# Performance work log

Hardware: AMD Instinct MI355X
Metric: run time of the kernel (lower is better)

## Reference

```python
import jax, jax.numpy as jnp
import numpy as np

MUL = 32          # multiplicity of 0e and 1o in edge_messages_irreps
E = 40000         # number of edges
NODE_DIM = 128    # 128x0e node feats
EDGE_DIM = 32     # 32x0e edge feats
WEIGHT_NUMEL = 5 * MUL * MUL  # 5 uvu instructions, (u,v)=(32,32) weights each

# Levi-Civita tensor = sqrt(6) * wigner_3j(1,1,1) in the e3nn real basis
_eps = np.zeros((3, 3, 3), np.float32)
for a, b, c in [(0, 1, 2), (1, 2, 0), (2, 0, 1)]:
    _eps[a, b, c] = 1.0
    _eps[a, c, b] = -1.0
EPS = jnp.asarray(_eps)


def setup_inputs() -> dict:
    key = jax.random.key(0)
    ks = jax.random.split(key, 13)
    return {
        "edge_feats": jax.random.normal(ks[0], (E, EDGE_DIM), jnp.float32),
        "edge_messages1": jax.random.normal(ks[1], (E, 4 * MUL), jnp.float32),
        "edge_messages2": jax.random.normal(ks[2], (E, 4 * MUL), jnp.float32),
        "node_feats_sender": jax.random.normal(ks[3], (E, NODE_DIM), jnp.float32),
        "node_feats_receiver": jax.random.normal(ks[4], (E, NODE_DIM), jnp.float32),
        "W_nodes": jax.random.normal(ks[5], (NODE_DIM, EDGE_DIM), jnp.float32),
        "W_mlp1": jax.random.normal(ks[6], (3 * EDGE_DIM, 128), jnp.float32),
        "W_mlp2": jax.random.normal(ks[7], (128, 128), jnp.float32),
        "W_mlp3": jax.random.normal(ks[8], (128, WEIGHT_NUMEL), jnp.float32),
        "W_out_0e": jax.random.normal(ks[9], (2 * MUL, MUL), jnp.float32),
        "W_out_1o": jax.random.normal(ks[10], (2 * MUL, MUL), jnp.float32),
        "W_out_1e": jax.random.normal(ks[11], (MUL, MUL), jnp.float32),
        "edge_index": jax.random.randint(ks[12], (2, E), 0, 10000, jnp.int64 if jax.config.jax_enable_x64 else jnp.int32),
    }


def reference(edge_feats, edge_messages1, edge_messages2, node_feats_sender,
              node_feats_receiver, W_nodes, W_mlp1, W_mlp2, W_mlp3,
              W_out_0e, W_out_1o, W_out_1e, edge_index):
    # nodes_linear: o3.Linear on pure scalars == dense matmul with 1/sqrt(fan_in)
    s_send = (node_feats_sender @ W_nodes) * (1.0 / np.sqrt(NODE_DIM))
    s_recv = (node_feats_receiver @ W_nodes) * (1.0 / np.sqrt(NODE_DIM))
    scal = jnp.concatenate([s_send, s_recv, edge_feats], axis=1)  # [E, 96]

    # FullyConnectedNet [96,128,128,weight_numel] with SiLU, e3nn fan-in scaling
    h = jax.nn.silu((scal @ W_mlp1) * (1.0 / np.sqrt(3 * EDGE_DIM)))
    h = jax.nn.silu((h @ W_mlp2) * (1.0 / np.sqrt(128)))
    w = (h @ W_mlp3) * (1.0 / np.sqrt(128))          # [E, 5120] per-edge TP weights
    w = w.reshape(-1, 5, MUL, MUL)                    # 5 uvu instructions

    # split messages into 32x0e scalars and 32x1o vectors
    x1_0 = edge_messages1[:, :MUL]
    x1_1 = edge_messages1[:, MUL:].reshape(-1, MUL, 3)
    x2_0 = edge_messages2[:, :MUL]
    x2_1 = edge_messages2[:, MUL:].reshape(-1, MUL, 3)

    # per-edge-weighted uvu tensor product; alpha = sqrt(ir_out.dim / fan) with
    # CG constants (1, d/sqrt(3), eps/sqrt(6)) folded in
    c1 = jnp.einsum('euv,eu,ev->eu', w[:, 0], x1_0, x2_0) * (1.0 / np.sqrt(MUL))          # 0e
    c2 = jnp.einsum('euv,eu,evj->euj', w[:, 1], x1_0, x2_1) * (1.0 / np.sqrt(MUL))        # 1o
    c3 = jnp.einsum('euv,eui,ev->eui', w[:, 2], x1_1, x2_0) * (1.0 / np.sqrt(MUL))        # 1o
    c4 = jnp.einsum('euv,eui,evi->eu', w[:, 3], x1_1, x2_1) * (1.0 / np.sqrt(3 * MUL))    # 0e
    c5 = jnp.einsum('euv,eui,evj,ijk->euk', w[:, 4], x1_1, x2_1, EPS) * (1.0 / np.sqrt(2 * MUL))  # 1e

    # output_linear: o3.Linear over irreps_mid -> 32x0e + 32x1o + 32x1e
    mid_0e = jnp.concatenate([c1, c4], axis=1)        # [E, 64]
    mid_1o = jnp.concatenate([c2, c3], axis=1)        # [E, 64, 3]
    out_0e = (mid_0e @ W_out_0e) * (1.0 / np.sqrt(2 * MUL))                      # [E, 32]
    out_1o = jnp.einsum('euj,uw->ewj', mid_1o, W_out_1o) * (1.0 / np.sqrt(2 * MUL))
    out_1e = jnp.einsum('euk,uw->ewk', c5, W_out_1e) * (1.0 / np.sqrt(MUL))

    n = out_0e.shape[0]
    return jnp.concatenate(
        [out_0e, out_1o.reshape(n, 3 * MUL), out_1e.reshape(n, 3 * MUL)], axis=1)  # [E, 224]
```

## Files before the change

kernel.cpp:

```cpp
#include <hip/hip_runtime.h>
#include <hip/hip_bf16.h>
#include <math.h>

typedef __attribute__((ext_vector_type(8)))  short bf16x8;
typedef __attribute__((ext_vector_type(4)))  float f32x4;
typedef __attribute__((ext_vector_type(16))) float f32x16;

#define S128 0.08838834764831845f
#define S96  0.10206207261596575f
#define S32  0.17677669529663687f
#define S64  0.125f
#define NE   40000

__device__ __forceinline__ float silu_f(float x){ return x / (1.0f + expf(-x)); }
__device__ __forceinline__ ushort f2b(float x){
    __hip_bfloat16 b = __float2bfloat16(x); return *(ushort*)&b;
}
__device__ __forceinline__ float b2f(ushort u){
    return __uint_as_float(((uint)u) << 16);
}
__device__ __forceinline__ uint packbf(float a, float b){
    return (uint)f2b(a) | ((uint)f2b(b) << 16);
}

__global__ __launch_bounds__(256)
void prep_weights(const float* __restrict__ Wn, const float* __restrict__ W1,
                  const float* __restrict__ W2, ushort* __restrict__ WnT,
                  ushort* __restrict__ W1T, ushort* __restrict__ W2T) {
    int idx = blockIdx.x * 256 + threadIdx.x;
    if (idx < 4096) {
        int n = idx >> 7, k = idx & 127;
        WnT[n * 128 + k] = f2b(Wn[k * 32 + n]);
    } else if (idx < 16384) {
        int t = idx - 4096; int n = t / 96, k = t - n * 96;
        W1T[n * 96 + k] = f2b(W1[k * 128 + n]);
    } else {
        int t = idx - 16384; int n = t >> 7, k = t & 127;
        W2T[n * 128 + k] = f2b(W2[k * 128 + n]);
    }
}

__global__ __launch_bounds__(256)
void w3_fragpack(const float* __restrict__ W3, ushort* __restrict__ w3A) {
    const int pu = blockIdx.x;
    const int t  = threadIdx.x;
    #pragma unroll
    for (int s = 0; s < 2; ++s) {
        int slot = s * 256 + t;
        int ks = slot >> 6, l = slot & 63;
        int m = pu * 32 + (l & 31);
        int kbase = ks * 16 + (l >> 5) * 8;
        bf16x8 v;
        #pragma unroll
        for (int i = 0; i < 8; ++i)
            v[i] = (short)f2b(W3[(size_t)(kbase + i) * 5120 + m]);
        *(bf16x8*)&w3A[((size_t)(pu * 8 + ks) * 64 + l) * 8] = v;
    }
}

__global__ __launch_bounds__(512, 6)
void mega6(const float* __restrict__ ef,  const float* __restrict__ em2,
           const float* __restrict__ nfs, const float* __restrict__ nfr,
           const ushort* __restrict__ WnT, const ushort* __restrict__ W1T,
           const ushort* __restrict__ W2T, const ushort* __restrict__ w3A,
           ushort* __restrict__ dt)
{
    __shared__ __align__(16) ushort scratch[16640];
    __shared__ __align__(16) ushort hbuf[64 * 128];

    const int tid  = threadIdx.x;
    const int lane = tid & 63, wv = tid >> 6;
    const int l15  = lane & 15, lg = lane >> 4;
    const int e0   = blockIdx.x * 64;

    ushort* scal = scratch;
    ushort* h1b  = scratch + 6656;
    float*  x2f  = (float*)scratch;

    #pragma unroll
    for (int q = 0; q < 4; ++q) {
        int idx = q * 512 + tid;
        int e = idx >> 5, j = idx & 31;
        scal[e * 104 + 64 + j] = f2b(ef[(size_t)(e0 + e) * 32 + j]);
    }

    {
        const int h = wv >> 2, eb = (wv & 3) * 16;
        const float* src = h ? nfr : nfs;
        const size_t erow = (size_t)(e0 + eb + l15) * 128;
        f32x4 acc1[2] = {{0,0,0,0},{0,0,0,0}};
        #pragma unroll
        for (int ks = 0; ks < 4; ++ks) {
            float4 va = *(const float4*)(src + erow + ks * 32 + lg * 8);
            float4 vb = *(const float4*)(src + erow + ks * 32 + lg * 8 + 4);
            bf16x8 a;
            a[0]=(short)f2b(va.x); a[1]=(short)f2b(va.y);
            a[2]=(short)f2b(va.z); a[3]=(short)f2b(va.w);
            a[4]=(short)f2b(vb.x); a[5]=(short)f2b(vb.y);
            a[6]=(short)f2b(vb.z); a[7]=(short)f2b(vb.w);
            #pragma unroll
            for (int nf = 0; nf < 2; ++nf) {
                bf16x8 b = *(const bf16x8*)(WnT + (nf * 16 + l15) * 128 + ks * 32 + lg * 8);
                acc1[nf] = __builtin_amdgcn_mfma_f32_16x16x32_bf16(a, b, acc1[nf], 0, 0, 0);
            }
        }
        #pragma unroll
        for (int nf = 0; nf < 2; ++nf)
            #pragma unroll
            for (int r = 0; r < 4; ++r)
                scal[(eb + lg * 4 + r) * 104 + h * 32 + nf * 16 + l15] =
                    f2b(acc1[nf][r] * S128);
    }
    __syncthreads();

    {
        const int et = wv & 3, nh = wv >> 2;
        f32x4 acc2[4] = {{0,0,0,0},{0,0,0,0},{0,0,0,0},{0,0,0,0}};
        #pragma unroll
        for (int ks = 0; ks < 3; ++ks) {
            bf16x8 a = *(const bf16x8*)&scal[(et * 16 + l15) * 104 + ks * 32 + lg * 8];
            #pragma unroll
            for (int nf = 0; nf < 4; ++nf) {
                int gn = nh * 4 + nf;
                bf16x8 b = *(const bf16x8*)(W1T + (gn * 16 + l15) * 96 + ks * 32 + lg * 8);
                acc2[nf] = __builtin_amdgcn_mfma_f32_16x16x32_bf16(a, b, acc2[nf], 0, 0, 0);
            }
        }
        #pragma unroll
        for (int nf = 0; nf < 4; ++nf)
            #pragma unroll
            for (int r = 0; r < 4; ++r)
                h1b[(et * 16 + lg * 4 + r) * 136 + (nh * 4 + nf) * 16 + l15] =
                    f2b(silu_f(acc2[nf][r] * S96));
    }
    __syncthreads();

    {
        const int et = wv & 3, nh = wv >> 2;
        f32x4 acc3[4] = {{0,0,0,0},{0,0,0,0},{0,0,0,0},{0,0,0,0}};
        #pragma unroll
        for (int ks = 0; ks < 4; ++ks) {
            bf16x8 a = *(const bf16x8*)&h1b[(et * 16 + l15) * 136 + ks * 32 + lg * 8];
            #pragma unroll
            for (int nf = 0; nf < 4; ++nf) {
                int gn = nh * 4 + nf;
                bf16x8 b = *(const bf16x8*)(W2T + (gn * 16 + l15) * 128 + ks * 32 + lg * 8);
                acc3[nf] = __builtin_amdgcn_mfma_f32_16x16x32_bf16(a, b, acc3[nf], 0, 0, 0);
            }
        }
        __syncthreads();
        #pragma unroll
        for (int nf = 0; nf < 4; ++nf)
            #pragma unroll
            for (int r = 0; r < 4; ++r) {
                int e = et * 16 + lg * 4 + r;
                int col = (nh * 4 + nf) * 16 + l15;
                hbuf[e * 128 + (col ^ ((e & 15) << 3))] =
                    f2b(silu_f(acc3[nf][r] * S128));
            }
    }

    {
        int e = tid >> 3, grp = tid & 7;
        const float* xr = em2 + (size_t)(e0 + e) * 128;
        float* dst = &x2f[e * 130];
        #pragma unroll
        for (int r = 0; r < 16; ++r) {
            int idx = grp * 16 + r;
            int reg = idx & 15;
            int vb = (reg & 3) + 8 * (reg >> 2);
            float val;
            if (idx < 32) {
                int hi2 = idx >> 4;
                val = xr[vb + 4 * hi2];
            } else {
                int slot = (idx - 32) >> 4;
                int j = slot >> 1, hi2 = slot & 1;
                val = xr[32 + (vb + 4 * hi2) * 3 + j];
            }
            dst[idx] = val;
        }
    }
    __syncthreads();

    const int el  = lane & 31;
    const int hi  = lane >> 5;
    const int sw0 = (el & 15) << 3;
    const float* x2r0 = &x2f[el * 130];
    const float* x2r1 = &x2f[(32 + el) * 130];

    #pragma unroll 1
    for (int un = 0; un < 20; ++un) {
        const int pu = un * 8 + wv;
        const int p = pu >> 5, u = pu & 31;
        const ushort* Ab = w3A + (size_t)pu * 4096 + lane * 8;

        bf16x8 a[8];
        #pragma unroll
        for (int ks = 0; ks < 8; ++ks)
            a[ks] = *(const bf16x8*)(Ab + ks * 512);

        #pragma unroll 1
        for (int eh = 0; eh < 2; ++eh) {
            const ushort* hrow = &hbuf[(eh * 32 + el) * 128];
            f32x16 acc = {0,0,0,0,0,0,0,0,0,0,0,0,0,0,0,0};
            #pragma unroll
            for (int ks = 0; ks < 8; ++ks) {
                bf16x8 b = *(const bf16x8*)&hrow[(ks * 16 + hi * 8) ^ sw0];
                acc = __builtin_amdgcn_mfma_f32_32x32x16_bf16(a[ks], b, acc, 0, 0, 0);
            }
            const float* xr = eh ? x2r1 : x2r0;
            const int ecol = e0 + eh * 32 + el;
            if (p == 0 || p == 2) {
                float s = 0.f;
                #pragma unroll
                for (int g = 0; g < 8; ++g) {
                    float2 q = *(const float2*)&xr[hi * 16 + g * 2];
                    s += acc[2*g] * q.x + acc[2*g+1] * q.y;
                }
                s += __shfl_xor(s, 32);
                if (hi == 0)
                    dt[(size_t)(((p == 0) ? 0 : 128) + u) * NE + ecol] = f2b(s * S128);
            } else {
                const int row0 = ((p == 1) ? 32 : (p == 3) ? 160 : 256) + u * 3;
                #pragma unroll
                for (int j = 0; j < 3; ++j) {
                    float s = 0.f;
                    #pragma unroll
                    for (int g = 0; g < 8; ++g) {
                        float2 q = *(const float2*)&xr[32 + (j * 2 + hi) * 16 + g * 2];
                        s += acc[2*g] * q.x + acc[2*g+1] * q.y;
                    }
                    s += __shfl_xor(s, 32);
                    if (hi == 0)
                        dt[(size_t)(row0 + j) * NE + ecol] = f2b(s * S128);
                }
            }
        }
    }
}

__global__ __launch_bounds__(256)
void finalize2(const float* __restrict__ em1, const ushort* __restrict__ dt,
               const float* __restrict__ W0e, const float* __restrict__ W1o,
               const float* __restrict__ W1e, float* __restrict__ out)
{
    __shared__ __align__(16) ushort dl[352 * 33];
    __shared__ __align__(16) ushort x1b[32 * 132];
    const int tid  = threadIdx.x;
    const int lane = tid & 63, wv = tid >> 6;
    const int l15  = lane & 15, lg = lane >> 4;
    const int eb   = blockIdx.x * 32;

    for (int idx = tid; idx < 352 * 32; idx += 256) {
        int row = idx >> 5, e = idx & 31;
        dl[row * 33 + e] = dt[(size_t)row * NE + eb + e];
    }
    {
        int e = tid >> 3, seg = tid & 7;
        const float* x1 = em1 + (size_t)(eb + e) * 128 + seg * 16;
        #pragma unroll
        for (int q = 0; q < 4; ++q) {
            float4 v = *(const float4*)(x1 + q * 4);
            *(uint*)&x1b[e * 132 + seg * 16 + q * 4]     = packbf(v.x, v.y);
            *(uint*)&x1b[e * 132 + seg * 16 + q * 4 + 2] = packbf(v.z, v.w);
        }
    }
    __syncthreads();

    #pragma unroll 1
    for (int it = 0; it < 4; ++it) {
        int unit = it * 4 + wv;
        if (unit >= 14) break;
        int mi = unit & 1, task = unit >> 1;
        const int ei = mi * 16 + l15;
        const ushort* xe = &x1b[ei * 132];
        const size_t orow = (size_t)(eb + mi * 16 + lg * 4) * 224;

        if (task == 0) {
            bf16x8 af0, af1;
            #pragma unroll
            for (int t = 0; t < 8; ++t) {
                int u = lg * 8 + t;
                af0[t] = (short)f2b(S32 * b2f(xe[u]) * b2f(dl[u * 33 + ei]));
                float c4 = 0.f;
                #pragma unroll
                for (int i = 0; i < 3; ++i)
                    c4 += b2f(xe[32 + u * 3 + i]) * b2f(dl[(160 + u * 3 + i) * 33 + ei]);
                af1[t] = (short)f2b(c4 * S96);
            }
            #pragma unroll
            for (int nf = 0; nf < 2; ++nf) {
                bf16x8 bf0, bf1;
                #pragma unroll
                for (int t = 0; t < 8; ++t) {
                    bf0[t] = (short)f2b(W0e[(lg * 8 + t) * 32 + nf * 16 + l15]);
                    bf1[t] = (short)f2b(W0e[(32 + lg * 8 + t) * 32 + nf * 16 + l15]);
                }
                f32x4 o = {0.f, 0.f, 0.f, 0.f};
                o = __builtin_amdgcn_mfma_f32_16x16x32_bf16(af0, bf0, o, 0, 0, 0);
                o = __builtin_amdgcn_mfma_f32_16x16x32_bf16(af1, bf1, o, 0, 0, 0);
                #pragma unroll
                for (int rr = 0; rr < 4; ++rr)
                    out[orow + (size_t)rr * 224 + nf * 16 + l15] = o[rr] * S64;
            }
        } else if (task <= 3) {
            int j = task - 1;
            bf16x8 af0, af1;
            #pragma unroll
            for (int t = 0; t < 8; ++t) {
                int u = lg * 8 + t;
                af0[t] = (short)f2b(S32 * b2f(xe[u]) * b2f(dl[(32 + u * 3 + j) * 33 + ei]));
                af1[t] = (short)f2b(S32 * b2f(xe[32 + u * 3 + j]) * b2f(dl[(128 + u) * 33 + ei]));
            }
            #pragma unroll
            for (int nf = 0; nf < 2; ++nf) {
                bf16x8 bf0, bf1;
                #pragma unroll
                for (int t = 0; t < 8; ++t) {
                    bf0[t] = (short)f2b(W1o[(lg * 8 + t) * 32 + nf * 16 + l15]);
                    bf1[t] = (short)f2b(W1o[(32 + lg * 8 + t) * 32 + nf * 16 + l15]);
                }
                f32x4 o = {0.f, 0.f, 0.f, 0.f};
                o = __builtin_amdgcn_mfma_f32_16x16x32_bf16(af0, bf0, o, 0, 0, 0);
                o = __builtin_amdgcn_mfma_f32_16x16x32_bf16(af1, bf1, o, 0, 0, 0);
                #pragma unroll
                for (int rr = 0; rr < 4; ++rr)
                    out[orow + (size_t)rr * 224 + 32 + (nf * 16 + l15) * 3 + j] = o[rr] * S64;
            }
        } else {
            int k = task - 4;
            int k1 = k + 1; if (k1 > 2) k1 -= 3;
            int k2 = k + 2; if (k2 > 2) k2 -= 3;
            bf16x8 af0;
            #pragma unroll
            for (int t = 0; t < 8; ++t) {
                int u = lg * 8 + t;
                float a_ = b2f(xe[32 + u * 3 + k1]) * b2f(dl[(256 + u * 3 + k2) * 33 + ei])
                         - b2f(xe[32 + u * 3 + k2]) * b2f(dl[(256 + u * 3 + k1) * 33 + ei]);
                af0[t] = (short)f2b(a_ * S64);
            }
            #pragma unroll
            for (int nf = 0; nf < 2; ++nf) {
                bf16x8 bf0;
                #pragma unroll
                for (int t = 0; t < 8; ++t)
                    bf0[t] = (short)f2b(W1e[(lg * 8 + t) * 32 + nf * 16 + l15]);
                f32x4 o = {0.f, 0.f, 0.f, 0.f};
                o = __builtin_amdgcn_mfma_f32_16x16x32_bf16(af0, bf0, o, 0, 0, 0);
                #pragma unroll
                for (int rr = 0; rr < 4; ++rr)
                    out[orow + (size_t)rr * 224 + 128 + (nf * 16 + l15) * 3 + k] = o[rr] * S32;
            }
        }
    }
}

extern "C" void kernel_launch(void* const* d_in, const int* in_sizes, int n_in,
                              void* d_out, int out_size, void* d_ws, size_t ws_size,
                              hipStream_t stream) {
    const float* ef  = (const float*)d_in[0];
    const float* em1 = (const float*)d_in[1];
    const float* em2 = (const float*)d_in[2];
    const float* nfs = (const float*)d_in[3];
    const float* nfr = (const float*)d_in[4];
    const float* Wn  = (const float*)d_in[5];
    const float* W1  = (const float*)d_in[6];
    const float* W2  = (const float*)d_in[7];
    const float* W3  = (const float*)d_in[8];
    const float* W0e = (const float*)d_in[9];
    const float* W1o = (const float*)d_in[10];
    const float* W1e = (const float*)d_in[11];
    float* out = (float*)d_out;

    const int E = in_sizes[0] / 32;

    char* ws = (char*)d_ws;
    ushort* w3A = (ushort*)ws;
    size_t off = (size_t)5120 * 128 * 2;
    ushort* WnT = (ushort*)(ws + off);  off += 32 * 128 * 2;
    ushort* W1T = (ushort*)(ws + off);  off += 128 * 96 * 2;
    ushort* W2T = (ushort*)(ws + off);  off += 128 * 128 * 2;
    ushort* dt  = (ushort*)(ws + off);

    prep_weights<<<128, 256, 0, stream>>>(Wn, W1, W2, WnT, W1T, W2T);
    w3_fragpack<<<160, 256, 0, stream>>>(W3, w3A);
    mega6<<<E / 64, 512, 0, stream>>>(ef, em2, nfs, nfr,
                                      WnT, W1T, W2T, w3A, dt);
    finalize2<<<E / 32, 256, 0, stream>>>(em1, dt, W0e, W1o, W1e, out);
}
```

Baseline: 145.0 us.

## Split fused MLP+W3 kernel into two kernels, doubling blocks for the W3 GEMM

The fused kernel is split into an MLP kernel that writes the per-tile h2 activations to a global scratch image, and a GEMM kernel launched with twice as many blocks, each handling half of the 160 (path,u) slices. The S128 scale is folded into the packed W3 weights, and the x2 contraction uses float4 LDS reads with a padded row stride. This aims to raise parallelism and shorten the serial per-block loop, at the cost of an extra global round trip for h2, a recomputed x2 staging per half, and an extra launch.

```diff
diff --git a/kernel.cpp b/kernel.cpp
--- a/kernel.cpp
+++ b/kernel.cpp
@@ -53,29 +53,28 @@
         bf16x8 v;
         #pragma unroll
         for (int i = 0; i < 8; ++i)
-            v[i] = (short)f2b(W3[(size_t)(kbase + i) * 5120 + m]);
+            v[i] = (short)f2b(W3[(size_t)(kbase + i) * 5120 + m] * S128);
         *(bf16x8*)&w3A[((size_t)(pu * 8 + ks) * 64 + l) * 8] = v;
     }
 }
 
 __global__ __launch_bounds__(512, 6)
-void mega6(const float* __restrict__ ef,  const float* __restrict__ em2,
-           const float* __restrict__ nfs, const float* __restrict__ nfr,
-           const ushort* __restrict__ WnT, const ushort* __restrict__ W1T,
-           const ushort* __restrict__ W2T, const ushort* __restrict__ w3A,
-           ushort* __restrict__ dt)
+void mlp_h2(const float* __restrict__ ef,  const float* __restrict__ nfs,
+            const float* __restrict__ nfr, const ushort* __restrict__ WnT,
+            const ushort* __restrict__ W1T, const ushort* __restrict__ W2T,
+            ushort* __restrict__ h2img)
 {
-    __shared__ __align__(16) ushort scratch[16640];
-    __shared__ __align__(16) ushort hbuf[64 * 128];
+    __shared__ __align__(16) ushort scratch[15360];
+    __shared__ __align__(16) ushort h2s[64 * 128];
 
     const int tid  = threadIdx.x;
     const int lane = tid & 63, wv = tid >> 6;
     const int l15  = lane & 15, lg = lane >> 4;
-    const int e0   = blockIdx.x * 64;
+    const int tile = blockIdx.x;
+    const int e0   = tile * 64;
 
     ushort* scal = scratch;
     ushort* h1b  = scratch + 6656;
-    float*  x2f  = (float*)scratch;
 
     #pragma unroll
     for (int q = 0; q < 4; ++q) {
@@ -148,22 +147,49 @@
                 acc3[nf] = __builtin_amdgcn_mfma_f32_16x16x32_bf16(a, b, acc3[nf], 0, 0, 0);
             }
         }
-        __syncthreads();
         #pragma unroll
         for (int nf = 0; nf < 4; ++nf)
             #pragma unroll
             for (int r = 0; r < 4; ++r) {
                 int e = et * 16 + lg * 4 + r;
                 int col = (nh * 4 + nf) * 16 + l15;
-                hbuf[e * 128 + (col ^ ((e & 15) << 3))] =
+                h2s[e * 128 + (col ^ ((e & 15) << 3))] =
                     f2b(silu_f(acc3[nf][r] * S128));
             }
     }
-
+    __syncthreads();
+
+    #pragma unroll
+    for (int it = 0; it < 2; ++it) {
+        int idx = it * 512 + tid;
+        *(bf16x8*)(h2img + (size_t)tile * 8192 + idx * 8) =
+            *(const bf16x8*)&h2s[idx * 8];
+    }
+}
+
+__global__ __launch_bounds__(512, 6)
+void gemm2(const float* __restrict__ em2, const ushort* __restrict__ w3A,
+           const ushort* __restrict__ h2img, ushort* __restrict__ dt)
+{
+    __shared__ __align__(16) ushort hbuf[64 * 128];
+    __shared__ __align__(16) float  x2f[64 * 132];
+
+    const int tid  = threadIdx.x;
+    const int lane = tid & 63, wv = tid >> 6;
+    const int tile = blockIdx.x >> 1;
+    const int half = blockIdx.x & 1;
+    const int e0   = tile * 64;
+
+    #pragma unroll
+    for (int it = 0; it < 2; ++it) {
+        int idx = it * 512 + tid;
+        *(bf16x8*)&hbuf[idx * 8] =
+            *(const bf16x8*)(h2img + (size_t)tile * 8192 + idx * 8);
+    }
     {
         int e = tid >> 3, grp = tid & 7;
         const float* xr = em2 + (size_t)(e0 + e) * 128;
-        float* dst = &x2f[e * 130];
+        float* dst = &x2f[e * 132];
         #pragma unroll
         for (int r = 0; r < 16; ++r) {
             int idx = grp * 16 + r;
@@ -186,12 +212,12 @@
     const int el  = lane & 31;
     const int hi  = lane >> 5;
     const int sw0 = (el & 15) << 3;
-    const float* x2r0 = &x2f[el * 130];
-    const float* x2r1 = &x2f[(32 + el) * 130];
+    const float* x2r0 = &x2f[el * 132];
+    const float* x2r1 = &x2f[(32 + el) * 132];
 
     #pragma unroll 1
-    for (int un = 0; un < 20; ++un) {
-        const int pu = un * 8 + wv;
+    for (int un = 0; un < 10; ++un) {
+        const int pu = half * 80 + un * 8 + wv;
         const int p = pu >> 5, u = pu & 31;
         const ushort* Ab = w3A + (size_t)pu * 4096 + lane * 8;
 
@@ -214,26 +240,28 @@
             if (p == 0 || p == 2) {
                 float s = 0.f;
                 #pragma unroll
-                for (int g = 0; g < 8; ++g) {
-                    float2 q = *(const float2*)&xr[hi * 16 + g * 2];
-                    s += acc[2*g] * q.x + acc[2*g+1] * q.y;
+                for (int g4 = 0; g4 < 4; ++g4) {
+                    float4 q = *(const float4*)&xr[hi * 16 + g4 * 4];
+                    s += acc[4*g4]*q.x + acc[4*g4+1]*q.y
+                       + acc[4*g4+2]*q.z + acc[4*g4+3]*q.w;
                 }
                 s += __shfl_xor(s, 32);
                 if (hi == 0)
-                    dt[(size_t)(((p == 0) ? 0 : 128) + u) * NE + ecol] = f2b(s * S128);
+                    dt[(size_t)(((p == 0) ? 0 : 128) + u) * NE + ecol] = f2b(s);
             } else {
                 const int row0 = ((p == 1) ? 32 : (p == 3) ? 160 : 256) + u * 3;
                 #pragma unroll
                 for (int j = 0; j < 3; ++j) {
                     float s = 0.f;
                     #pragma unroll
-                    for (int g = 0; g < 8; ++g) {
-                        float2 q = *(const float2*)&xr[32 + (j * 2 + hi) * 16 + g * 2];
-                        s += acc[2*g] * q.x + acc[2*g+1] * q.y;
+                    for (int g4 = 0; g4 < 4; ++g4) {
+                        float4 q = *(const float4*)&xr[32 + (j * 2 + hi) * 16 + g4 * 4];
+                        s += acc[4*g4]*q.x + acc[4*g4+1]*q.y
+                           + acc[4*g4+2]*q.z + acc[4*g4+3]*q.w;
                     }
                     s += __shfl_xor(s, 32);
                     if (hi == 0)
-                        dt[(size_t)(row0 + j) * NE + ecol] = f2b(s * S128);
+                        dt[(size_t)(row0 + j) * NE + ecol] = f2b(s);
                 }
             }
         }
@@ -381,11 +409,12 @@
     ushort* WnT = (ushort*)(ws + off);  off += 32 * 128 * 2;
     ushort* W1T = (ushort*)(ws + off);  off += 128 * 96 * 2;
     ushort* W2T = (ushort*)(ws + off);  off += 128 * 128 * 2;
-    ushort* dt  = (ushort*)(ws + off);
+    ushort* dt  = (ushort*)(ws + off);  off += (size_t)352 * E * 2;
+    ushort* h2img = (ushort*)(ws + off);
 
     prep_weights<<<128, 256, 0, stream>>>(Wn, W1, W2, WnT, W1T, W2T);
     w3_fragpack<<<160, 256, 0, stream>>>(W3, w3A);
-    mega6<<<E / 64, 512, 0, stream>>>(ef, em2, nfs, nfr,
-                                      WnT, W1T, W2T, w3A, dt);
+    mlp_h2<<<E / 64, 512, 0, stream>>>(ef, nfs, nfr, WnT, W1T, W2T, h2img);
+    gemm2<<<2 * (E / 64), 512, 0, stream>>>(em2, w3A, h2img, dt);
     finalize2<<<E / 32, 256, 0, stream>>>(em1, dt, W0e, W1o, W1e, out);
 }
```

Result: slower. 170.1 us (+17.3%).
